# Optimization experiments

Measured on AMD Instinct MI355X. Metric: run time of the kernel, lower is better.

The kernel has to match this reference:

```python
import jax, jax.numpy as jnp
import numpy as np

N_NODES = 100000
N_EDGES = 1600000
N_GRAPHS = 512
X_DIM = 4
H = 64
L = 3
NUM_CLASS = 3


def setup_inputs() -> dict:
    key = jax.random.key(0)
    ks = jax.random.split(key, 16)
    s = 0.1
    return {
        "x": jax.random.normal(ks[0], (N_NODES, X_DIM), jnp.float32),
        "edge_index": jax.random.randint(ks[1], (2, N_EDGES), 0, N_NODES, jnp.int64),
        "batch": jnp.sort(jax.random.randint(ks[2], (N_NODES,), 0, N_GRAPHS, jnp.int64)),
        "edge_attr": jax.random.uniform(ks[3], (N_EDGES,), jnp.float32),
        # node embedding
        "W_emb": jax.random.normal(ks[4], (X_DIM, H), jnp.float32) * s,
        "b_emb": jnp.zeros((H,), jnp.float32),
        # LEConv per-layer params (stacked over layers)
        "W1": jax.random.normal(ks[5], (L, H, H), jnp.float32) * s,
        "b1": jnp.zeros((L, H), jnp.float32),
        "W2": jax.random.normal(ks[6], (L, H, H), jnp.float32) * s,  # no bias (lin2)
        "W3": jax.random.normal(ks[7], (L, H, H), jnp.float32) * s,
        "b3": jnp.zeros((L, H), jnp.float32),
        # fc_out head
        "Wf1": jax.random.normal(ks[8], (H, 2 * H), jnp.float32) * s,
        "bf1": jnp.zeros((2 * H,), jnp.float32),
        "Wf2": jax.random.normal(ks[9], (2 * H, NUM_CLASS), jnp.float32) * s,
        "bf2": jnp.zeros((NUM_CLASS,), jnp.float32),
    }


def reference(x, edge_index, batch, edge_attr, W_emb, b_emb, W1, b1, W2, W3, b3,
              Wf1, bf1, Wf2, bf2):
    src, dst = edge_index[0], edge_index[1]
    # node embedding
    h = x @ W_emb + b_emb  # [N, H]
    # stacked LEConv layers: x_i' = sum_{j->i} e_ji * (lin1(x_j) - lin2(x_i)) + lin3(x_i)
    for l in range(L):
        a = h @ W1[l] + b1[l]          # [N, H]
        b = h @ W2[l]                  # [N, H] (lin2 has no bias)
        msg = (a[src] - b[dst]) * edge_attr[:, None]  # [E, H]
        agg = jax.ops.segment_sum(msg, dst, num_segments=N_NODES)
        h = jax.nn.relu(agg + h @ W3[l] + b3[l])
    # global mean pool per graph
    sums = jax.ops.segment_sum(h, batch, num_segments=N_GRAPHS)  # [G, H]
    cnt = jax.ops.segment_sum(jnp.ones((N_NODES,), h.dtype), batch, num_segments=N_GRAPHS)
    graph_x = sums / jnp.maximum(cnt, 1.0)[:, None]
    # fc_out head
    hid = jax.nn.relu(graph_x @ Wf1 + bf1)
    return hid @ Wf2 + bf2  # [G, NUM_CLASS]
```

## Files before the change

kernel.cpp:

```cpp
#include <hip/hip_runtime.h>

#define N_NODES 100000
#define N_EDGES 1600000
#define N_GRAPHS 512
#define X_DIM 4
#define H 64
#define LAYERS 3
#define NUM_CLASS 3
#define NBLK 256
#define EPB (N_EDGES / NBLK)
#define BKT_BITS 9
#define BKT_SZ 512
#define NBKT ((N_NODES + BKT_SZ - 1) / BKT_SZ)
#define MHIST (NBKT * NBLK)
#define LROW 72
#define NCHUNKS ((N_NODES + 63) / 64)

typedef unsigned short ushort;
typedef short bf16x8 __attribute__((ext_vector_type(8)));
typedef unsigned short ush8 __attribute__((ext_vector_type(8)));
typedef float floatx4 __attribute__((ext_vector_type(4)));

__device__ __forceinline__ ushort f2bf(float v) {
    unsigned u = __float_as_uint(v);
    unsigned r = (u + 0x7fff + ((u >> 16) & 1)) >> 16;
    return (ushort)r;
}
__device__ __forceinline__ float bf2f(ushort s) {
    return __uint_as_float(((unsigned)s) << 16);
}

__global__ void precomp_kernel(const float* __restrict__ Wemb, const float* __restrict__ bemb,
                               const float* __restrict__ W1, const float* __restrict__ b1,
                               const float* __restrict__ W2, const float* __restrict__ W3,
                               const float* __restrict__ b3,
                               float* __restrict__ G, float* __restrict__ C) {
    int f = threadIdx.x;
    if (f >= H) return;
    const float* Ws[3] = {W1, W2, W3};
#pragma unroll
    for (int wsel = 0; wsel < 3; ++wsel) {
        const float* W = Ws[wsel];
#pragma unroll
        for (int c = 0; c < X_DIM; ++c) {
            float g = 0.f;
            for (int k = 0; k < H; ++k) g += Wemb[c * H + k] * W[k * H + f];
            G[wsel * 256 + c * H + f] = g;
        }
        float cb = (wsel == 0) ? b1[f] : (wsel == 2) ? b3[f] : 0.f;
        for (int k = 0; k < H; ++k) cb += bemb[k] * W[k * H + f];
        C[wsel * H + f] = cb;
    }
}

__global__ __launch_bounds__(256) void hist1_kernel(const int* __restrict__ dst,
                                                    int* __restrict__ histM) {
    __shared__ int hist[NBKT];
    int t = threadIdx.x, b = blockIdx.x;
    for (int i = t; i < NBKT; i += 256) hist[i] = 0;
    __syncthreads();
    int e0 = b * EPB;
    for (int j = t; j < EPB; j += 256) {
        int d = dst[e0 + j];
        atomicAdd(hist + (d >> BKT_BITS), 1);
    }
    __syncthreads();
    for (int i = t; i < NBKT; i += 256) histM[i * NBLK + b] = hist[i];
}

__global__ __launch_bounds__(512) void gscan1_kernel(const int* __restrict__ v,
                                                     int* __restrict__ incl,
                                                     int* __restrict__ partials) {
    __shared__ int s[512];
    int tid = threadIdx.x;
    int i = blockIdx.x * 512 + tid;
    int x = (i < MHIST) ? v[i] : 0;
    s[tid] = x;
    for (int off = 1; off < 512; off <<= 1) {
        __syncthreads();
        int tv = (tid >= off) ? s[tid - off] : 0;
        __syncthreads();
        s[tid] += tv;
    }
    __syncthreads();
    if (i < MHIST) incl[i] = s[tid];
    if (tid == 511) partials[blockIdx.x] = s[tid];
}

__global__ __launch_bounds__(512) void gscan2_kernel(const int* __restrict__ partials,
                                                     int* __restrict__ chunk_off, int nchunk) {
    __shared__ int s[512];
    int tid = threadIdx.x;
    s[tid] = (tid < nchunk) ? partials[tid] : 0;
    for (int off = 1; off < 512; off <<= 1) {
        __syncthreads();
        int tv = (tid >= off) ? s[tid - off] : 0;
        __syncthreads();
        s[tid] += tv;
    }
    __syncthreads();
    int excl = (tid == 0) ? 0 : s[tid - 1];
    __syncthreads();
    if (tid < nchunk) chunk_off[tid] = excl;
}

__global__ void gscan3_kernel(const int* __restrict__ v, const int* __restrict__ incl,
                              const int* __restrict__ chunk_off,
                              int* __restrict__ ebase, int* __restrict__ bkt_ptr) {
    int i = blockIdx.x * 256 + threadIdx.x;
    if (i >= MHIST) return;
    int e = incl[i] + chunk_off[i >> 9] - v[i];
    ebase[i] = e;
    if ((i & (NBLK - 1)) == 0) bkt_ptr[i / NBLK] = e;
    if (i == MHIST - 1) bkt_ptr[NBKT] = e + v[i];
}

__global__ __launch_bounds__(256) void scatter1_kernel(
    const int* __restrict__ src, const int* __restrict__ dst, const float* __restrict__ ea,
    const int* __restrict__ ebase, unsigned* __restrict__ eb_se, int* __restrict__ eb_dst) {
    __shared__ int cur[NBKT];
    int t = threadIdx.x, b = blockIdx.x;
    for (int i = t; i < NBKT; i += 256) cur[i] = ebase[i * NBLK + b];
    __syncthreads();
    int e0 = b * EPB;
    for (int j = t; j < EPB; j += 256) {
        int e = e0 + j;
        int d = dst[e];
        int k = d >> BKT_BITS;
        int pos = atomicAdd(cur + k, 1);
        eb_se[pos] = ((unsigned)src[e] << 15) | (unsigned)f2bf(ea[e]);
        eb_dst[pos] = d;
    }
}

__global__ __launch_bounds__(512) void bucket_kernel(
    const int* __restrict__ bkt_ptr, const unsigned* __restrict__ eb_se,
    const int* __restrict__ eb_dst,
    int* __restrict__ row_ptr, float* __restrict__ degw, unsigned* __restrict__ epack) {
    __shared__ int cnt[BKT_SZ];
    __shared__ float dws[BKT_SZ];
    __shared__ int s[BKT_SZ];
    __shared__ int cur[BKT_SZ];
    int k = blockIdx.x, t = threadIdx.x;
    int base = k << BKT_BITS;
    int nn = N_NODES - base;
    if (nn > BKT_SZ) nn = BKT_SZ;
    cnt[t] = 0;
    dws[t] = 0.0f;
    __syncthreads();
    int beg = bkt_ptr[k], end = bkt_ptr[k + 1];
    for (int j = beg + t; j < end; j += 512) {
        int d = eb_dst[j] - base;
        atomicAdd(cnt + d, 1);
        atomicAdd(dws + d, __uint_as_float((eb_se[j] & 0x7FFFu) << 16));
    }
    __syncthreads();
    s[t] = cnt[t];
    for (int off = 1; off < 512; off <<= 1) {
        __syncthreads();
        int tv = (t >= off) ? s[t - off] : 0;
        __syncthreads();
        s[t] += tv;
    }
    __syncthreads();
    int rstart = beg + s[t] - cnt[t];
    if (t < nn) {
        row_ptr[base + t] = rstart;
        degw[base + t] = dws[t];
        cur[t] = rstart;
    }
    __syncthreads();
    for (int j = beg + t; j < end; j += 512) {
        unsigned se = eb_se[j];
        int d = eb_dst[j] - base;
        int pos = atomicAdd(cur + d, 1);
        epack[pos] = se;
    }
    if (k == NBKT - 1 && t == 0) row_ptr[N_NODES] = N_EDGES;
}

__global__ __launch_bounds__(256) void xgather_kernel(
    const int* __restrict__ row_ptr, const unsigned* __restrict__ epack,
    const float* __restrict__ x, float* __restrict__ mx) {
    int n = blockIdx.x * 4 + (threadIdx.x >> 6);
    if (n >= N_NODES) return;
    int lane = threadIdx.x & 63;
    int q = lane >> 1, cp = lane & 1;
    int beg = row_ptr[n], end = row_ptr[n + 1];
    float a0 = 0.f, a1 = 0.f;
    for (int j = beg; j < end; j += 32) {
        int jk = j + q;
        unsigned w = (jk < end) ? epack[jk] : 0u;
        float2 xv = *(const float2*)&x[(size_t)(w >> 15) * X_DIM + cp * 2];
        float e = __uint_as_float((w & 0x7FFFu) << 16);
        a0 += e * xv.x;
        a1 += e * xv.y;
    }
#pragma unroll
    for (int mask = 2; mask <= 32; mask <<= 1) {
        a0 += __shfl_xor(a0, mask);
        a1 += __shfl_xor(a1, mask);
    }
    if (lane < 2) {
        mx[(size_t)n * X_DIM + lane * 2] = a0;
        mx[(size_t)n * X_DIM + lane * 2 + 1] = a1;
    }
}

__global__ void combine_kernel(const float* __restrict__ x, const float* __restrict__ mx,
                               const float* __restrict__ degw,
                               const float* __restrict__ G, const float* __restrict__ C,
                               ushort* __restrict__ h) {
    int i = blockIdx.x * blockDim.x + threadIdx.x;
    if (i >= N_NODES * H) return;
    int n = i >> 6, f = i & 63;
    floatx4 xv = *(const floatx4*)&x[(size_t)n * X_DIM];
    floatx4 mv = *(const floatx4*)&mx[(size_t)n * X_DIM];
    float dw = degw[n];
    float t1 = mv[0] * G[f] + mv[1] * G[64 + f] + mv[2] * G[128 + f] + mv[3] * G[192 + f];
    float t2 = xv[0] * G[256 + f] + xv[1] * G[320 + f] + xv[2] * G[384 + f] + xv[3] * G[448 + f];
    float t3 = xv[0] * G[512 + f] + xv[1] * G[576 + f] + xv[2] * G[640 + f] + xv[3] * G[704 + f];
    float v = t1 + dw * C[f] + t3 + C[128 + f] - (t2 + C[64 + f]) * dw;
    h[i] = f2bf(fmaxf(v, 0.0f));
}

__global__ __launch_bounds__(256) void gather_kernel(
    const int* __restrict__ row_ptr, const unsigned* __restrict__ epack,
    const ushort* __restrict__ h, ushort* __restrict__ m) {
    int n = blockIdx.x * 4 + (threadIdx.x >> 6);
    if (n >= N_NODES) return;
    int lane = threadIdx.x & 63;
    int q = lane >> 3, s = lane & 7;
    int beg = row_ptr[n], end = row_ptr[n + 1];
    float acc[8] = {0.f, 0.f, 0.f, 0.f, 0.f, 0.f, 0.f, 0.f};
    for (int j = beg; j < end; j += 32) {
        unsigned w[4];
#pragma unroll
        for (int k = 0; k < 4; ++k) {
            int jk = j + k * 8 + q;
            w[k] = (jk < end) ? epack[jk] : 0u;
        }
        ush8 av[4];
#pragma unroll
        for (int k = 0; k < 4; ++k)
            av[k] = *(const ush8*)&h[(size_t)(w[k] >> 15) * H + s * 8];
#pragma unroll
        for (int k = 0; k < 4; ++k) {
            float e = __uint_as_float((w[k] & 0x7FFFu) << 16);
#pragma unroll
            for (int i = 0; i < 8; ++i)
                acc[i] += e * bf2f((ushort)av[k][i]);
        }
    }
#pragma unroll
    for (int i = 0; i < 8; ++i) {
        acc[i] += __shfl_xor(acc[i], 8);
        acc[i] += __shfl_xor(acc[i], 16);
        acc[i] += __shfl_xor(acc[i], 32);
    }
    if (q == 0) {
        ush8 r;
#pragma unroll
        for (int i = 0; i < 8; ++i) r[i] = (short)f2bf(acc[i]);
        *(ush8*)&m[(size_t)n * H + s * 8] = r;
    }
}

__global__ __launch_bounds__(256) void linC_kernel(
    ushort* __restrict__ h, const ushort* __restrict__ m,
    const float* __restrict__ degw,
    const float* __restrict__ W1, const float* __restrict__ bias1,
    const float* __restrict__ W2, const float* __restrict__ W3,
    const float* __restrict__ bias3) {
    __shared__ alignas(16) ushort ah[64 * LROW];
    __shared__ alignas(16) ushort am[64 * LROW];
    int t = threadIdx.x;
    int wv = t >> 6, lane = t & 63;
    int quad = lane >> 4, m16 = lane & 15;
    int f = wv * 16 + m16;
    bf16x8 B[3][2][2];
    const float* Ws[3] = {W1, W2, W3};
#pragma unroll
    for (int wsel = 0; wsel < 3; ++wsel) {
#pragma unroll
        for (int kh = 0; kh < 2; ++kh) {
#pragma unroll
            for (int j = 0; j < 8; ++j) {
                float w = Ws[wsel][(kh * 32 + quad * 8 + j) * H + f];
                ushort hi = f2bf(w);
                B[wsel][kh][0][j] = (short)hi;
                B[wsel][kh][1][j] = (short)f2bf(w - bf2f(hi));
            }
        }
    }
    float bb1 = bias1[f], bb3 = bias3[f];
    for (int chunk = blockIdx.x; chunk < NCHUNKS; chunk += gridDim.x) {
        int nbase = chunk * 64;
        __syncthreads();
        for (int v = t; v < 64 * 8; v += 256) {
            int nl = v >> 3, k0 = (v & 7) * 8;
            int n = nbase + nl;
            ush8 vh = {0, 0, 0, 0, 0, 0, 0, 0};
            ush8 vm = {0, 0, 0, 0, 0, 0, 0, 0};
            if (n < N_NODES) {
                vh = *(const ush8*)&h[(size_t)n * H + k0];
                vm = *(const ush8*)&m[(size_t)n * H + k0];
            }
            *(ush8*)&ah[nl * LROW + k0] = vh;
            *(ush8*)&am[nl * LROW + k0] = vm;
        }
        __syncthreads();
#pragma unroll
        for (int ng = 0; ng < 4; ++ng) {
            int abase = (ng * 16 + m16) * LROW + quad * 8;
            bf16x8 Ah0 = *(const bf16x8*)&ah[abase];
            bf16x8 Ah1 = *(const bf16x8*)&ah[abase + 32];
            bf16x8 Am0 = *(const bf16x8*)&am[abase];
            bf16x8 Am1 = *(const bf16x8*)&am[abase + 32];
            floatx4 acc1 = {0.f, 0.f, 0.f, 0.f};
            floatx4 acc2 = {0.f, 0.f, 0.f, 0.f};
            floatx4 acc3 = {0.f, 0.f, 0.f, 0.f};
            acc1 = __builtin_amdgcn_mfma_f32_16x16x32_bf16(Am0, B[0][0][0], acc1, 0, 0, 0);
            acc1 = __builtin_amdgcn_mfma_f32_16x16x32_bf16(Am0, B[0][0][1], acc1, 0, 0, 0);
            acc1 = __builtin_amdgcn_mfma_f32_16x16x32_bf16(Am1, B[0][1][0], acc1, 0, 0, 0);
            acc1 = __builtin_amdgcn_mfma_f32_16x16x32_bf16(Am1, B[0][1][1], acc1, 0, 0, 0);
            acc2 = __builtin_amdgcn_mfma_f32_16x16x32_bf16(Ah0, B[1][0][0], acc2, 0, 0, 0);
            acc2 = __builtin_amdgcn_mfma_f32_16x16x32_bf16(Ah0, B[1][0][1], acc2, 0, 0, 0);
            acc2 = __builtin_amdgcn_mfma_f32_16x16x32_bf16(Ah1, B[1][1][0], acc2, 0, 0, 0);
            acc2 = __builtin_amdgcn_mfma_f32_16x16x32_bf16(Ah1, B[1][1][1], acc2, 0, 0, 0);
            acc3 = __builtin_amdgcn_mfma_f32_16x16x32_bf16(Ah0, B[2][0][0], acc3, 0, 0, 0);
            acc3 = __builtin_amdgcn_mfma_f32_16x16x32_bf16(Ah0, B[2][0][1], acc3, 0, 0, 0);
            acc3 = __builtin_amdgcn_mfma_f32_16x16x32_bf16(Ah1, B[2][1][0], acc3, 0, 0, 0);
            acc3 = __builtin_amdgcn_mfma_f32_16x16x32_bf16(Ah1, B[2][1][1], acc3, 0, 0, 0);
            int nrow = nbase + ng * 16 + quad * 4;
#pragma unroll
            for (int r = 0; r < 4; ++r) {
                int n = nrow + r;
                if (n < N_NODES) {
                    float dw = degw[n];
                    float v = acc1[r] + dw * bb1 + acc3[r] + bb3 - acc2[r] * dw;
                    h[(size_t)n * H + f] = f2bf(fmaxf(v, 0.0f));
                }
            }
        }
    }
}

__device__ __forceinline__ int lower_bound(const int* __restrict__ arr, int n, int key) {
    int lo = 0, hi = n;
    while (lo < hi) {
        int mid = (lo + hi) >> 1;
        if (arr[mid] < key) lo = mid + 1; else hi = mid;
    }
    return lo;
}

__global__ __launch_bounds__(256) void poolhead_kernel(
    const ushort* __restrict__ h, const int* __restrict__ batch,
    const float* __restrict__ Wf1, const float* __restrict__ bf1v,
    const float* __restrict__ Wf2, const float* __restrict__ bf2v,
    float* __restrict__ out) {
    __shared__ float psum[4][H];
    __shared__ float gx[H];
    __shared__ float hid[2 * H];
    int g = blockIdx.x, t = threadIdx.x;
    int s = lower_bound(batch, N_NODES, g);
    int e = lower_bound(batch, N_NODES, g + 1);
    int lane = t & 63, wv = t >> 6;
    int o = lane & 7;
    int nd = t >> 3;
    float acc[8] = {0.f, 0.f, 0.f, 0.f, 0.f, 0.f, 0.f, 0.f};
    for (int n = s + nd; n < e; n += 32) {
        ush8 v = *(const ush8*)&h[(size_t)n * H + o * 8];
#pragma unroll
        for (int i = 0; i < 8; ++i) acc[i] += bf2f((ushort)v[i]);
    }
#pragma unroll
    for (int i = 0; i < 8; ++i) {
        acc[i] += __shfl_xor(acc[i], 8);
        acc[i] += __shfl_xor(acc[i], 16);
        acc[i] += __shfl_xor(acc[i], 32);
    }
    if (lane < 8) {
#pragma unroll
        for (int i = 0; i < 8; ++i) psum[wv][o * 8 + i] = acc[i];
    }
    __syncthreads();
    if (t < H) {
        float c = (float)(e - s);
        gx[t] = (psum[0][t] + psum[1][t] + psum[2][t] + psum[3][t]) / fmaxf(c, 1.0f);
    }
    __syncthreads();
    if (t < 2 * H) {
        float acc2 = bf1v[t];
        for (int k = 0; k < H; ++k) acc2 += gx[k] * Wf1[k * 2 * H + t];
        hid[t] = fmaxf(acc2, 0.0f);
    }
    __syncthreads();
    if (t < NUM_CLASS) {
        float o2 = bf2v[t];
        for (int k = 0; k < 2 * H; ++k) o2 += hid[k] * Wf2[k * NUM_CLASS + t];
        out[g * NUM_CLASS + t] = o2;
    }
}

extern "C" void kernel_launch(void* const* d_in, const int* in_sizes, int n_in,
                              void* d_out, int out_size, void* d_ws, size_t ws_size,
                              hipStream_t stream) {
    const float* x    = (const float*)d_in[0];
    const int*  ei    = (const int*)d_in[1];
    const int*  batch = (const int*)d_in[2];
    const float* ea   = (const float*)d_in[3];
    const float* Wemb = (const float*)d_in[4];
    const float* bemb = (const float*)d_in[5];
    const float* pW1  = (const float*)d_in[6];
    const float* pb1  = (const float*)d_in[7];
    const float* pW2  = (const float*)d_in[8];
    const float* pW3  = (const float*)d_in[9];
    const float* pb3  = (const float*)d_in[10];
    const float* Wf1  = (const float*)d_in[11];
    const float* bf1v = (const float*)d_in[12];
    const float* Wf2  = (const float*)d_in[13];
    const float* bf2v = (const float*)d_in[14];
    float* out = (float*)d_out;

    const int* src = ei;
    const int* dst = ei + N_EDGES;

    const size_t NH = (size_t)N_NODES * H;
    char* p = (char*)d_ws;
    ushort* h       = (ushort*)p;            p += NH * 2;
    ushort* m       = (ushort*)p;            p += NH * 2;
    float*  mx      = (float*)p;             p += (size_t)N_NODES * X_DIM * 4;
    unsigned* epack = (unsigned*)p;          p += (size_t)N_EDGES * 4;
    int*   histM    = (int*)p;               p += MHIST * 4;
    int*   incl     = (int*)p;               p += MHIST * 4;
    int*   ebase    = (int*)p;               p += MHIST * 4;
    int*   partials = (int*)p;               p += 512 * 4;
    int*   chunk_off= (int*)p;               p += 512 * 4;
    int*   bkt_ptr  = (int*)p;               p += (NBKT + 1) * 4;
    int*   row_ptr  = (int*)p;               p += (N_NODES + 1) * 4;
    float* degw     = (float*)p;             p += N_NODES * 4;
    float* Gbuf     = (float*)p;             p += 3 * 256 * 4;
    float* Cbuf     = (float*)p;             p += 3 * 64 * 4;
    unsigned* eb_se = (unsigned*)m;
    int*     eb_dst = (int*)h;

    precomp_kernel<<<1, 64, 0, stream>>>(Wemb, bemb, pW1, pb1, pW2, pW3, pb3, Gbuf, Cbuf);

    hist1_kernel<<<NBLK, 256, 0, stream>>>(dst, histM);
    gscan1_kernel<<<MHIST / 512, 512, 0, stream>>>(histM, incl, partials);
    gscan2_kernel<<<1, 512, 0, stream>>>(partials, chunk_off, MHIST / 512);
    gscan3_kernel<<<(MHIST + 255) / 256, 256, 0, stream>>>(histM, incl, chunk_off, ebase, bkt_ptr);
    scatter1_kernel<<<NBLK, 256, 0, stream>>>(src, dst, ea, ebase, eb_se, eb_dst);
    bucket_kernel<<<NBKT, 512, 0, stream>>>(bkt_ptr, eb_se, eb_dst, row_ptr, degw, epack);

    xgather_kernel<<<(N_NODES + 3) / 4, 256, 0, stream>>>(row_ptr, epack, x, mx);
    combine_kernel<<<(N_NODES * H + 255) / 256, 256, 0, stream>>>(x, mx, degw, Gbuf, Cbuf, h);

    for (int l = 1; l < LAYERS; ++l) {
        gather_kernel<<<(N_NODES + 3) / 4, 256, 0, stream>>>(row_ptr, epack, h, m);
        linC_kernel<<<512, 256, 0, stream>>>(
            h, m, degw,
            pW1 + (size_t)l * H * H, pb1 + (size_t)l * H,
            pW2 + (size_t)l * H * H,
            pW3 + (size_t)l * H * H, pb3 + (size_t)l * H);
    }

    poolhead_kernel<<<N_GRAPHS, 256, 0, stream>>>(h, batch, Wf1, bf1v, Wf2, bf2v, out);
}
```

Before: 331.9 us.

## Fuse small setup kernels into neighbours and merge first-layer gather with combine

```diff
diff --git a/kernel.cpp b/kernel.cpp
--- a/kernel.cpp
+++ b/kernel.cpp
@@ -13,6 +13,7 @@
 #define BKT_SZ 512
 #define NBKT ((N_NODES + BKT_SZ - 1) / BKT_SZ)
 #define MHIST (NBKT * NBLK)
+#define NCH (MHIST / 512)
 #define LROW 72
 #define NCHUNKS ((N_NODES + 63) / 64)
 
@@ -30,31 +31,13 @@
     return __uint_as_float(((unsigned)s) << 16);
 }
 
-__global__ void precomp_kernel(const float* __restrict__ Wemb, const float* __restrict__ bemb,
-                               const float* __restrict__ W1, const float* __restrict__ b1,
-                               const float* __restrict__ W2, const float* __restrict__ W3,
-                               const float* __restrict__ b3,
-                               float* __restrict__ G, float* __restrict__ C) {
-    int f = threadIdx.x;
-    if (f >= H) return;
-    const float* Ws[3] = {W1, W2, W3};
-#pragma unroll
-    for (int wsel = 0; wsel < 3; ++wsel) {
-        const float* W = Ws[wsel];
-#pragma unroll
-        for (int c = 0; c < X_DIM; ++c) {
-            float g = 0.f;
-            for (int k = 0; k < H; ++k) g += Wemb[c * H + k] * W[k * H + f];
-            G[wsel * 256 + c * H + f] = g;
-        }
-        float cb = (wsel == 0) ? b1[f] : (wsel == 2) ? b3[f] : 0.f;
-        for (int k = 0; k < H; ++k) cb += bemb[k] * W[k * H + f];
-        C[wsel * H + f] = cb;
-    }
-}
-
-__global__ __launch_bounds__(256) void hist1_kernel(const int* __restrict__ dst,
-                                                    int* __restrict__ histM) {
+__global__ __launch_bounds__(256) void hist1_kernel(
+    const int* __restrict__ dst, int* __restrict__ histM,
+    const float* __restrict__ Wemb, const float* __restrict__ bemb,
+    const float* __restrict__ W1, const float* __restrict__ b1,
+    const float* __restrict__ W2, const float* __restrict__ W3,
+    const float* __restrict__ b3,
+    float* __restrict__ G, float* __restrict__ C) {
     __shared__ int hist[NBKT];
     int t = threadIdx.x, b = blockIdx.x;
     for (int i = t; i < NBKT; i += 256) hist[i] = 0;
@@ -66,6 +49,23 @@
     }
     __syncthreads();
     for (int i = t; i < NBKT; i += 256) histM[i * NBLK + b] = hist[i];
+    if (b == 0 && t < H) {
+        int f = t;
+        const float* Ws[3] = {W1, W2, W3};
+#pragma unroll
+        for (int wsel = 0; wsel < 3; ++wsel) {
+            const float* W = Ws[wsel];
+#pragma unroll
+            for (int c = 0; c < X_DIM; ++c) {
+                float g = 0.f;
+                for (int k = 0; k < H; ++k) g += Wemb[c * H + k] * W[k * H + f];
+                G[wsel * 256 + c * H + f] = g;
+            }
+            float cb = (wsel == 0) ? b1[f] : (wsel == 2) ? b3[f] : 0.f;
+            for (int k = 0; k < H; ++k) cb += bemb[k] * W[k * H + f];
+            C[wsel * H + f] = cb;
+        }
+    }
 }
 
 __global__ __launch_bounds__(512) void gscan1_kernel(const int* __restrict__ v,
@@ -87,41 +87,33 @@
     if (tid == 511) partials[blockIdx.x] = s[tid];
 }
 
-__global__ __launch_bounds__(512) void gscan2_kernel(const int* __restrict__ partials,
-                                                     int* __restrict__ chunk_off, int nchunk) {
-    __shared__ int s[512];
-    int tid = threadIdx.x;
-    s[tid] = (tid < nchunk) ? partials[tid] : 0;
-    for (int off = 1; off < 512; off <<= 1) {
-        __syncthreads();
-        int tv = (tid >= off) ? s[tid - off] : 0;
-        __syncthreads();
-        s[tid] += tv;
-    }
-    __syncthreads();
-    int excl = (tid == 0) ? 0 : s[tid - 1];
-    __syncthreads();
-    if (tid < nchunk) chunk_off[tid] = excl;
-}
-
-__global__ void gscan3_kernel(const int* __restrict__ v, const int* __restrict__ incl,
-                              const int* __restrict__ chunk_off,
-                              int* __restrict__ ebase, int* __restrict__ bkt_ptr) {
-    int i = blockIdx.x * 256 + threadIdx.x;
-    if (i >= MHIST) return;
-    int e = incl[i] + chunk_off[i >> 9] - v[i];
-    ebase[i] = e;
-    if ((i & (NBLK - 1)) == 0) bkt_ptr[i / NBLK] = e;
-    if (i == MHIST - 1) bkt_ptr[NBKT] = e + v[i];
-}
-
 __global__ __launch_bounds__(256) void scatter1_kernel(
     const int* __restrict__ src, const int* __restrict__ dst, const float* __restrict__ ea,
-    const int* __restrict__ ebase, unsigned* __restrict__ eb_se, int* __restrict__ eb_dst) {
+    const int* __restrict__ histM, const int* __restrict__ incl,
+    const int* __restrict__ partials,
+    unsigned* __restrict__ eb_se, int* __restrict__ eb_dst, int* __restrict__ bkt_ptr) {
+    __shared__ int coff[128];
     __shared__ int cur[NBKT];
     int t = threadIdx.x, b = blockIdx.x;
-    for (int i = t; i < NBKT; i += 256) cur[i] = ebase[i * NBLK + b];
-    __syncthreads();
+    if (t < 128) coff[t] = (t < NCH) ? partials[t] : 0;
+    __syncthreads();
+    for (int off = 1; off < 128; off <<= 1) {
+        int tv = (t < 128 && t >= off) ? coff[t - off] : 0;
+        __syncthreads();
+        if (t < 128) coff[t] += tv;
+        __syncthreads();
+    }
+    for (int i = t; i < NBKT; i += 256) {
+        int idx = i * NBLK + b;
+        int ch = idx >> 9;
+        int off0 = (ch == 0) ? 0 : coff[ch - 1];
+        cur[i] = incl[idx] - histM[idx] + off0;
+    }
+    __syncthreads();
+    if (b == 0) {
+        for (int i = t; i < NBKT; i += 256) bkt_ptr[i] = cur[i];
+        if (t == 0) bkt_ptr[NBKT] = N_EDGES;
+    }
     int e0 = b * EPB;
     for (int j = t; j < EPB; j += 256) {
         int e = e0 + j;
@@ -179,17 +171,24 @@
     if (k == NBKT - 1 && t == 0) row_ptr[N_NODES] = N_EDGES;
 }
 
-__global__ __launch_bounds__(256) void xgather_kernel(
+__global__ __launch_bounds__(256) void layer1_kernel(
     const int* __restrict__ row_ptr, const unsigned* __restrict__ epack,
-    const float* __restrict__ x, float* __restrict__ mx) {
+    const float* __restrict__ x, const float* __restrict__ degw,
+    const float* __restrict__ G, const float* __restrict__ C,
+    ushort* __restrict__ h) {
     int n = blockIdx.x * 4 + (threadIdx.x >> 6);
     if (n >= N_NODES) return;
     int lane = threadIdx.x & 63;
-    int q = lane >> 1, cp = lane & 1;
+    float Gr[12], Cr[3];
+#pragma unroll
+    for (int i = 0; i < 12; ++i) Gr[i] = G[(i >> 2) * 256 + (i & 3) * 64 + lane];
+#pragma unroll
+    for (int i = 0; i < 3; ++i) Cr[i] = C[i * 64 + lane];
+    int q2 = lane >> 1, cp = lane & 1;
     int beg = row_ptr[n], end = row_ptr[n + 1];
     float a0 = 0.f, a1 = 0.f;
     for (int j = beg; j < end; j += 32) {
-        int jk = j + q;
+        int jk = j + q2;
         unsigned w = (jk < end) ? epack[jk] : 0u;
         float2 xv = *(const float2*)&x[(size_t)(w >> 15) * X_DIM + cp * 2];
         float e = __uint_as_float((w & 0x7FFFu) << 16);
@@ -201,27 +200,15 @@
         a0 += __shfl_xor(a0, mask);
         a1 += __shfl_xor(a1, mask);
     }
-    if (lane < 2) {
-        mx[(size_t)n * X_DIM + lane * 2] = a0;
-        mx[(size_t)n * X_DIM + lane * 2 + 1] = a1;
-    }
-}
-
-__global__ void combine_kernel(const float* __restrict__ x, const float* __restrict__ mx,
-                               const float* __restrict__ degw,
-                               const float* __restrict__ G, const float* __restrict__ C,
-                               ushort* __restrict__ h) {
-    int i = blockIdx.x * blockDim.x + threadIdx.x;
-    if (i >= N_NODES * H) return;
-    int n = i >> 6, f = i & 63;
-    floatx4 xv = *(const floatx4*)&x[(size_t)n * X_DIM];
-    floatx4 mv = *(const floatx4*)&mx[(size_t)n * X_DIM];
+    float mv0 = __shfl(a0, 0), mv1 = __shfl(a1, 0);
+    float mv2 = __shfl(a0, 1), mv3 = __shfl(a1, 1);
+    floatx4 xr = *(const floatx4*)&x[(size_t)n * X_DIM];
     float dw = degw[n];
-    float t1 = mv[0] * G[f] + mv[1] * G[64 + f] + mv[2] * G[128 + f] + mv[3] * G[192 + f];
-    float t2 = xv[0] * G[256 + f] + xv[1] * G[320 + f] + xv[2] * G[384 + f] + xv[3] * G[448 + f];
-    float t3 = xv[0] * G[512 + f] + xv[1] * G[576 + f] + xv[2] * G[640 + f] + xv[3] * G[704 + f];
-    float v = t1 + dw * C[f] + t3 + C[128 + f] - (t2 + C[64 + f]) * dw;
-    h[i] = f2bf(fmaxf(v, 0.0f));
+    float t1 = mv0 * Gr[0] + mv1 * Gr[1] + mv2 * Gr[2] + mv3 * Gr[3];
+    float t2 = xr[0] * Gr[4] + xr[1] * Gr[5] + xr[2] * Gr[6] + xr[3] * Gr[7];
+    float t3 = xr[0] * Gr[8] + xr[1] * Gr[9] + xr[2] * Gr[10] + xr[3] * Gr[11];
+    float v = t1 + dw * Cr[0] + t3 + Cr[2] - (t2 + Cr[1]) * dw;
+    h[(size_t)n * H + lane] = f2bf(fmaxf(v, 0.0f));
 }
 
 __global__ __launch_bounds__(256) void gather_kernel(
@@ -431,13 +418,10 @@
     char* p = (char*)d_ws;
     ushort* h       = (ushort*)p;            p += NH * 2;
     ushort* m       = (ushort*)p;            p += NH * 2;
-    float*  mx      = (float*)p;             p += (size_t)N_NODES * X_DIM * 4;
     unsigned* epack = (unsigned*)p;          p += (size_t)N_EDGES * 4;
     int*   histM    = (int*)p;               p += MHIST * 4;
     int*   incl     = (int*)p;               p += MHIST * 4;
-    int*   ebase    = (int*)p;               p += MHIST * 4;
     int*   partials = (int*)p;               p += 512 * 4;
-    int*   chunk_off= (int*)p;               p += 512 * 4;
     int*   bkt_ptr  = (int*)p;               p += (NBKT + 1) * 4;
     int*   row_ptr  = (int*)p;               p += (N_NODES + 1) * 4;
     float* degw     = (float*)p;             p += N_NODES * 4;
@@ -446,17 +430,15 @@
     unsigned* eb_se = (unsigned*)m;
     int*     eb_dst = (int*)h;
 
-    precomp_kernel<<<1, 64, 0, stream>>>(Wemb, bemb, pW1, pb1, pW2, pW3, pb3, Gbuf, Cbuf);
-
-    hist1_kernel<<<NBLK, 256, 0, stream>>>(dst, histM);
+    hist1_kernel<<<NBLK, 256, 0, stream>>>(dst, histM, Wemb, bemb, pW1, pb1, pW2, pW3, pb3,
+                                           Gbuf, Cbuf);
     gscan1_kernel<<<MHIST / 512, 512, 0, stream>>>(histM, incl, partials);
-    gscan2_kernel<<<1, 512, 0, stream>>>(partials, chunk_off, MHIST / 512);
-    gscan3_kernel<<<(MHIST + 255) / 256, 256, 0, stream>>>(histM, incl, chunk_off, ebase, bkt_ptr);
-    scatter1_kernel<<<NBLK, 256, 0, stream>>>(src, dst, ea, ebase, eb_se, eb_dst);
+    scatter1_kernel<<<NBLK, 256, 0, stream>>>(src, dst, ea, histM, incl, partials,
+                                              eb_se, eb_dst, bkt_ptr);
     bucket_kernel<<<NBKT, 512, 0, stream>>>(bkt_ptr, eb_se, eb_dst, row_ptr, degw, epack);
 
-    xgather_kernel<<<(N_NODES + 3) / 4, 256, 0, stream>>>(row_ptr, epack, x, mx);
-    combine_kernel<<<(N_NODES * H + 255) / 256, 256, 0, stream>>>(x, mx, degw, Gbuf, Cbuf, h);
+    layer1_kernel<<<(N_NODES + 3) / 4, 256, 0, stream>>>(row_ptr, epack, x, degw,
+                                                         Gbuf, Cbuf, h);
 
     for (int l = 1; l < LAYERS; ++l) {
         gather_kernel<<<(N_NODES + 3) / 4, 256, 0, stream>>>(row_ptr, epack, h, m);
```

Result: faster. 315.4 us (-5.0%).
